# Optimization experiments

Hardware: AMD Instinct MI355X
Metric: run time of the kernel (lower is better)

Reference implementation:

```python
import jax, jax.numpy as jnp
import numpy as np


def ste_sign(x):
    # larq ste_sign forward: sign(x) with sign(0) = 1
    return jnp.where(x >= 0, 1.0, -1.0).astype(x.dtype)


def setup_inputs() -> dict:
    key = jax.random.key(0)
    ks = jax.random.split(key, 8)
    B, H, W, Cin, Cout = 32, 56, 56, 256, 256
    x = jax.random.normal(ks[0], (B, H, W, Cin), dtype=jnp.float32)
    bias1 = jax.random.normal(ks[1], (1, 1, 1, Cin), dtype=jnp.float32) * 0.01
    kernel = jax.random.normal(ks[2], (3, 3, Cin, Cout), dtype=jnp.float32) * 0.1
    # BatchNormalization(scale=False): beta learnable, gamma=1, moving stats
    bn_beta = jax.random.normal(ks[3], (Cout,), dtype=jnp.float32) * 0.01
    bn_mean = jax.random.normal(ks[4], (Cout,), dtype=jnp.float32) * 0.01
    bn_var = jax.random.uniform(ks[5], (Cout,), dtype=jnp.float32, minval=0.5, maxval=1.5)
    bias2 = jax.random.normal(ks[6], (1, 1, 1, Cout), dtype=jnp.float32) * 0.01
    return {"x": x, "bias1": bias1, "kernel": kernel, "bn_beta": bn_beta,
            "bn_mean": bn_mean, "bn_var": bn_var, "bias2": bias2}


def reference(x, bias1, kernel, bn_beta, bn_mean, bn_var, bias2):
    eps = 1e-3  # keras BatchNormalization default epsilon
    strides = 1
    # lb_activation_1: learnable bias + ste_sign activation
    a = ste_sign(x + bias1)
    # QuantConv2D: binarize kernel, 'same' padding conv (NHWC, HWIO)
    qk = ste_sign(kernel)
    y = jax.lax.conv_general_dilated(
        a, qk, window_strides=(strides, strides), padding='SAME',
        dimension_numbers=('NHWC', 'HWIO', 'NHWC'))
    # BatchNormalization(scale=False) inference: (y - mean)/sqrt(var+eps) + beta
    y = (y - bn_mean) * jax.lax.rsqrt(bn_var + eps) + bn_beta
    # strides == 1: no avgpool residual branch
    # lb_activation_2: learnable bias + relu
    out = jax.nn.relu(y + bias2)
    return out
```

## Files before the change

### kernel.cpp

```cpp
#include <hip/hip_runtime.h>


typedef int v4i __attribute__((ext_vector_type(4)));
typedef unsigned int u32;

#define NB   32
#define HW   56
#define HP   58
#define HP2  (HP*HP)
#define CIN  256
#define COUT 256
#define NPIX (NB*HW*HW)
#define KTOT 2304
#define BM   128
#define BN   256
#define NSTEP 36
#define NWG  (NPIX/BM)

#define PA_BYTES ((size_t)NB*HP*HP*CIN)
#define WT_OFF   PA_BYTES
#define WT_BYTES ((size_t)KTOT*COUT)
#define SC_OFF   (WT_OFF + WT_BYTES)
#define SH_OFF   (SC_OFF + 1024)

__device__ __forceinline__ void g2l16(const void* g, void* l) {
    __builtin_amdgcn_global_load_lds(
        (const __attribute__((address_space(1))) void*)g,
        (__attribute__((address_space(3))) void*)l, 16, 0, 0);
}

__global__ __launch_bounds__(256) void pack_a_kernel(
    const float* __restrict__ x, const float* __restrict__ b1,
    signed char* __restrict__ pa)
{
    const int lane = threadIdx.x & 63;
    const int pp = blockIdx.x * 4 + (threadIdx.x >> 6);
    const int n = pp / HP2, r = pp % HP2, ph = r / HP, pw = r % HP;
    const int ci = lane * 4;
    u32 o = 0;
    if (ph >= 1 && ph <= HW && pw >= 1 && pw <= HW) {
        const int pix = (n * HW + ph - 1) * HW + (pw - 1);
        const float4 xv = *(const float4*)(x + (size_t)pix * CIN + ci);
        const float4 bv = *(const float4*)(b1 + ci);
        o  = (u32)(unsigned char)((xv.x + bv.x >= 0.f) ? 1 : -1);
        o |= (u32)(unsigned char)((xv.y + bv.y >= 0.f) ? 1 : -1) << 8;
        o |= (u32)(unsigned char)((xv.z + bv.z >= 0.f) ? 1 : -1) << 16;
        o |= (u32)(unsigned char)((xv.w + bv.w >= 0.f) ? 1 : -1) << 24;
    }
    *(u32*)(pa + (size_t)pp * CIN + ci) = o;
}

__global__ __launch_bounds__(256) void packw_kernel(
    const float* __restrict__ k, signed char* __restrict__ wt)
{
    __shared__ signed char tile[64][256];
    const int t = threadIdx.x, k0 = blockIdx.x * 64;
    for (int j = 0; j < 64; ++j)
        tile[j][t] = (k[(size_t)(k0 + j) * COUT + t] >= 0.f) ? 1 : -1;
    __syncthreads();
    u32 wd[16];
#pragma unroll
    for (int j = 0; j < 16; ++j) wd[j] = 0;
#pragma unroll
    for (int j = 0; j < 64; ++j)
        wd[j >> 2] |= ((u32)(unsigned char)tile[j][t]) << ((j & 3) * 8);
    uint4* dst = (uint4*)(wt + (size_t)t * KTOT + k0);
#pragma unroll
    for (int j = 0; j < 4; ++j)
        dst[j] = make_uint4(wd[4*j], wd[4*j+1], wd[4*j+2], wd[4*j+3]);
}

__global__ __launch_bounds__(256) void bnprep_kernel(
    const float* __restrict__ beta, const float* __restrict__ mean,
    const float* __restrict__ var, const float* __restrict__ b2,
    float* __restrict__ scale, float* __restrict__ shift)
{
    const int t = threadIdx.x;
    const float s = rsqrtf(var[t] + 1e-3f);
    scale[t] = s;
    shift[t] = beta[t] - mean[t] * s + b2[t];
}

__global__ __launch_bounds__(256, 2) void conv_mfma_kernel(
    const signed char* __restrict__ pa, const signed char* __restrict__ wt,
    const float* __restrict__ scale, const float* __restrict__ shift,
    float* __restrict__ out)
{
    __shared__ signed char L[2][24576];

    const int t = threadIdx.x, l = t & 63, v = t >> 6;
    const int swz = (blockIdx.x & 7) * (NWG / 8) + (blockIdx.x >> 3);
    const int p0 = swz * BM;

    const signed char* abase[2];
#pragma unroll
    for (int i = 0; i < 2; ++i) {
        const int q = (t >> 2) + i * 64;
        const int p = p0 + q;
        const int n = p / 3136, r = p % 3136, h = r / 56, w = r % 56;
        const int aswz = (((t & 3) ^ ((q >> 1) & 3)) << 4);
        abase[i] = pa + ((size_t)(n * HP + h) * HP + w) * CIN + aswz;
    }
    const signed char* wbase[4];
#pragma unroll
    for (int j = 0; j < 4; ++j) {
        const int r = j * 64 + (t >> 2);
        const int bswz = (((t & 3) ^ ((r >> 1) & 3)) << 4);
        wbase[j] = wt + (size_t)r * KTOT + bswz;
    }

    int aoff[8], boff[4];
#pragma unroll
    for (int pg = 0; pg < 8; ++pg) {
        const int row = pg * 16 + (l & 15);
        aoff[pg] = row * 64 + ((((l >> 4) ^ (row >> 1)) & 3) << 4);
    }
#pragma unroll
    for (int cg = 0; cg < 4; ++cg) {
        const int row = v * 64 + cg * 16 + (l & 15);
        boff[cg] = 8192 + row * 64 + ((((l >> 4) ^ (row >> 1)) & 3) << 4);
    }

    v4i acc[8][4];
#pragma unroll
    for (int i = 0; i < 8; ++i)
#pragma unroll
        for (int j = 0; j < 4; ++j) acc[i][j] = (v4i){0, 0, 0, 0};

    auto goffA = [&](int s) {
        const int tap = s >> 2, cq = s & 3;
        const int ty = tap / 3, tx = tap - ty * 3;
        return ((ty * HP + tx) << 8) + (cq << 6);
    };
    auto STAGE = [&](int buf, int s) {
        const int go = goffA(s);
        g2l16(abase[0] + go, &L[buf][v * 1024]);
        g2l16(abase[1] + go, &L[buf][4096 + v * 1024]);
#pragma unroll
        for (int j = 0; j < 4; ++j)
            g2l16(wbase[j] + (s << 6), &L[buf][8192 + j * 4096 + v * 1024]);
    };

    STAGE(0, 0);
    asm volatile("s_waitcnt vmcnt(0)" ::: "memory");
    __builtin_amdgcn_s_barrier();

#pragma unroll 1
    for (int s = 0; s < NSTEP; ++s) {
        const int cur = s & 1, nxt = cur ^ 1;
        const signed char* Lc = &L[cur][0];
        if (s + 1 < NSTEP) STAGE(nxt, s + 1);
        v4i bf0 = *(const v4i*)(Lc + boff[0]);
        v4i bf1 = *(const v4i*)(Lc + boff[1]);
        v4i bf2 = *(const v4i*)(Lc + boff[2]);
        v4i bf3 = *(const v4i*)(Lc + boff[3]);
        v4i af[8];
#pragma unroll
        for (int pg = 0; pg < 8; ++pg) af[pg] = *(const v4i*)(Lc + aoff[pg]);
        __builtin_amdgcn_s_setprio(1);
#pragma unroll
        for (int pg = 0; pg < 8; ++pg) {
            acc[pg][0] = __builtin_amdgcn_mfma_i32_16x16x64_i8(af[pg], bf0, acc[pg][0], 0, 0, 0);
            acc[pg][1] = __builtin_amdgcn_mfma_i32_16x16x64_i8(af[pg], bf1, acc[pg][1], 0, 0, 0);
            acc[pg][2] = __builtin_amdgcn_mfma_i32_16x16x64_i8(af[pg], bf2, acc[pg][2], 0, 0, 0);
            acc[pg][3] = __builtin_amdgcn_mfma_i32_16x16x64_i8(af[pg], bf3, acc[pg][3], 0, 0, 0);
        }
        __builtin_amdgcn_s_setprio(0);
        asm volatile("s_waitcnt vmcnt(0)" ::: "memory");
        __builtin_amdgcn_s_barrier();
    }

#pragma unroll
    for (int cg = 0; cg < 4; ++cg) {
        const int co = v * 64 + cg * 16 + (l & 15);
        const float sc = scale[co], sh = shift[co];
#pragma unroll
        for (int pg = 0; pg < 8; ++pg) {
            const int prow0 = p0 + pg * 16 + (l >> 4) * 4;
#pragma unroll
            for (int rr = 0; rr < 4; ++rr) {
                const float y = (float)acc[pg][cg][rr];
                out[(size_t)(prow0 + rr) * COUT + co] = fmaxf(fmaf(y, sc, sh), 0.f);
            }
        }
    }
}

extern "C" void kernel_launch(void* const* d_in, const int* in_sizes, int n_in,
                              void* d_out, int out_size, void* d_ws, size_t ws_size,
                              hipStream_t stream)
{
    const float* x      = (const float*)d_in[0];
    const float* bias1  = (const float*)d_in[1];
    const float* kernel = (const float*)d_in[2];
    const float* bn_beta = (const float*)d_in[3];
    const float* bn_mean = (const float*)d_in[4];
    const float* bn_var  = (const float*)d_in[5];
    const float* bias2   = (const float*)d_in[6];
    float* out = (float*)d_out;

    signed char* pa  = (signed char*)d_ws;
    signed char* wtp = (signed char*)d_ws + WT_OFF;
    float* scale = (float*)((char*)d_ws + SC_OFF);
    float* shift = (float*)((char*)d_ws + SH_OFF);

    pack_a_kernel<<<dim3(NB * HP2 / 4), dim3(256), 0, stream>>>(x, bias1, pa);
    packw_kernel<<<dim3(KTOT / 64), dim3(256), 0, stream>>>(kernel, wtp);
    bnprep_kernel<<<dim3(1), dim3(256), 0, stream>>>(bn_beta, bn_mean, bn_var, bias2,
                                                     scale, shift);
    conv_mfma_kernel<<<dim3(NWG), dim3(256), 0, stream>>>(pa, wtp, scale, shift, out);
}
```

Measured before the change: 104.4 us.

## Enlarge conv tile to 256x256 with 8 waves and split MFMA phases with barriers

The implicit-GEMM conv workgroup now covers 256 pixels instead of 128 and uses 512 threads arranged as 2x4 waves. Each K-step stages twice as much A data and the same amount of weights into a larger LDS buffer, which halves per-pixel weight traffic. The MFMA loop is split into two halves separated by extra barriers so that LDS reads, the next-stage prefetch and MFMAs from different waves interleave. The costs are more barriers per step, fewer workgroups (392), and 64KB of LDS per block, which may limit occupancy.

```diff
diff --git a/kernel.cpp b/kernel.cpp
--- a/kernel.cpp
+++ b/kernel.cpp
@@ -12,7 +12,7 @@
 #define COUT 256
 #define NPIX (NB*HW*HW)
 #define KTOT 2304
-#define BM   128
+#define BM   256
 #define BN   256
 #define NSTEP 36
 #define NWG  (NPIX/BM)
@@ -81,30 +81,31 @@
     shift[t] = beta[t] - mean[t] * s + b2[t];
 }
 
-__global__ __launch_bounds__(256, 2) void conv_mfma_kernel(
+__global__ __launch_bounds__(512, 2) void conv_mfma_kernel(
     const signed char* __restrict__ pa, const signed char* __restrict__ wt,
     const float* __restrict__ scale, const float* __restrict__ shift,
     float* __restrict__ out)
 {
-    __shared__ signed char L[2][24576];
-
-    const int t = threadIdx.x, l = t & 63, v = t >> 6;
+    __shared__ signed char L[2][32768];
+
+    const int t = threadIdx.x, l = t & 63, w = t >> 6;
+    const int wr = w >> 2, wc = w & 3;
     const int swz = (blockIdx.x & 7) * (NWG / 8) + (blockIdx.x >> 3);
     const int p0 = swz * BM;
 
     const signed char* abase[2];
 #pragma unroll
     for (int i = 0; i < 2; ++i) {
-        const int q = (t >> 2) + i * 64;
+        const int q = (t >> 2) + i * 128;
         const int p = p0 + q;
-        const int n = p / 3136, r = p % 3136, h = r / 56, w = r % 56;
+        const int n = p / 3136, r = p % 3136, h = r / 56, ww = r % 56;
         const int aswz = (((t & 3) ^ ((q >> 1) & 3)) << 4);
-        abase[i] = pa + ((size_t)(n * HP + h) * HP + w) * CIN + aswz;
-    }
-    const signed char* wbase[4];
-#pragma unroll
-    for (int j = 0; j < 4; ++j) {
-        const int r = j * 64 + (t >> 2);
+        abase[i] = pa + ((size_t)(n * HP + h) * HP + ww) * CIN + aswz;
+    }
+    const signed char* wbase[2];
+#pragma unroll
+    for (int j = 0; j < 2; ++j) {
+        const int r = j * 128 + (t >> 2);
         const int bswz = (((t & 3) ^ ((r >> 1) & 3)) << 4);
         wbase[j] = wt + (size_t)r * KTOT + bswz;
     }
@@ -112,13 +113,13 @@
     int aoff[8], boff[4];
 #pragma unroll
     for (int pg = 0; pg < 8; ++pg) {
-        const int row = pg * 16 + (l & 15);
+        const int row = wr * 128 + pg * 16 + (l & 15);
         aoff[pg] = row * 64 + ((((l >> 4) ^ (row >> 1)) & 3) << 4);
     }
 #pragma unroll
     for (int cg = 0; cg < 4; ++cg) {
-        const int row = v * 64 + cg * 16 + (l & 15);
-        boff[cg] = 8192 + row * 64 + ((((l >> 4) ^ (row >> 1)) & 3) << 4);
+        const int row = wc * 64 + cg * 16 + (l & 15);
+        boff[cg] = 16384 + row * 64 + ((((l >> 4) ^ (row >> 1)) & 3) << 4);
     }
 
     v4i acc[8][4];
@@ -134,11 +135,10 @@
     };
     auto STAGE = [&](int buf, int s) {
         const int go = goffA(s);
-        g2l16(abase[0] + go, &L[buf][v * 1024]);
-        g2l16(abase[1] + go, &L[buf][4096 + v * 1024]);
-#pragma unroll
-        for (int j = 0; j < 4; ++j)
-            g2l16(wbase[j] + (s << 6), &L[buf][8192 + j * 4096 + v * 1024]);
+        g2l16(abase[0] + go, &L[buf][w * 1024]);
+        g2l16(abase[1] + go, &L[buf][8192 + w * 1024]);
+        g2l16(wbase[0] + (s << 6), &L[buf][16384 + w * 1024]);
+        g2l16(wbase[1] + (s << 6), &L[buf][24576 + w * 1024]);
     };
 
     STAGE(0, 0);
@@ -149,22 +149,62 @@
     for (int s = 0; s < NSTEP; ++s) {
         const int cur = s & 1, nxt = cur ^ 1;
         const signed char* Lc = &L[cur][0];
-        if (s + 1 < NSTEP) STAGE(nxt, s + 1);
+
         v4i bf0 = *(const v4i*)(Lc + boff[0]);
         v4i bf1 = *(const v4i*)(Lc + boff[1]);
         v4i bf2 = *(const v4i*)(Lc + boff[2]);
         v4i bf3 = *(const v4i*)(Lc + boff[3]);
-        v4i af[8];
-#pragma unroll
-        for (int pg = 0; pg < 8; ++pg) af[pg] = *(const v4i*)(Lc + aoff[pg]);
+        v4i af0 = *(const v4i*)(Lc + aoff[0]);
+        v4i af1 = *(const v4i*)(Lc + aoff[1]);
+        v4i af2 = *(const v4i*)(Lc + aoff[2]);
+        v4i af3 = *(const v4i*)(Lc + aoff[3]);
+        if (s + 1 < NSTEP) STAGE(nxt, s + 1);
+        asm volatile("" ::: "memory");
+        __builtin_amdgcn_s_barrier();
         __builtin_amdgcn_s_setprio(1);
-#pragma unroll
-        for (int pg = 0; pg < 8; ++pg) {
-            acc[pg][0] = __builtin_amdgcn_mfma_i32_16x16x64_i8(af[pg], bf0, acc[pg][0], 0, 0, 0);
-            acc[pg][1] = __builtin_amdgcn_mfma_i32_16x16x64_i8(af[pg], bf1, acc[pg][1], 0, 0, 0);
-            acc[pg][2] = __builtin_amdgcn_mfma_i32_16x16x64_i8(af[pg], bf2, acc[pg][2], 0, 0, 0);
-            acc[pg][3] = __builtin_amdgcn_mfma_i32_16x16x64_i8(af[pg], bf3, acc[pg][3], 0, 0, 0);
-        }
+        acc[0][0] = __builtin_amdgcn_mfma_i32_16x16x64_i8(af0, bf0, acc[0][0], 0, 0, 0);
+        acc[0][1] = __builtin_amdgcn_mfma_i32_16x16x64_i8(af0, bf1, acc[0][1], 0, 0, 0);
+        acc[0][2] = __builtin_amdgcn_mfma_i32_16x16x64_i8(af0, bf2, acc[0][2], 0, 0, 0);
+        acc[0][3] = __builtin_amdgcn_mfma_i32_16x16x64_i8(af0, bf3, acc[0][3], 0, 0, 0);
+        acc[1][0] = __builtin_amdgcn_mfma_i32_16x16x64_i8(af1, bf0, acc[1][0], 0, 0, 0);
+        acc[1][1] = __builtin_amdgcn_mfma_i32_16x16x64_i8(af1, bf1, acc[1][1], 0, 0, 0);
+        acc[1][2] = __builtin_amdgcn_mfma_i32_16x16x64_i8(af1, bf2, acc[1][2], 0, 0, 0);
+        acc[1][3] = __builtin_amdgcn_mfma_i32_16x16x64_i8(af1, bf3, acc[1][3], 0, 0, 0);
+        acc[2][0] = __builtin_amdgcn_mfma_i32_16x16x64_i8(af2, bf0, acc[2][0], 0, 0, 0);
+        acc[2][1] = __builtin_amdgcn_mfma_i32_16x16x64_i8(af2, bf1, acc[2][1], 0, 0, 0);
+        acc[2][2] = __builtin_amdgcn_mfma_i32_16x16x64_i8(af2, bf2, acc[2][2], 0, 0, 0);
+        acc[2][3] = __builtin_amdgcn_mfma_i32_16x16x64_i8(af2, bf3, acc[2][3], 0, 0, 0);
+        acc[3][0] = __builtin_amdgcn_mfma_i32_16x16x64_i8(af3, bf0, acc[3][0], 0, 0, 0);
+        acc[3][1] = __builtin_amdgcn_mfma_i32_16x16x64_i8(af3, bf1, acc[3][1], 0, 0, 0);
+        acc[3][2] = __builtin_amdgcn_mfma_i32_16x16x64_i8(af3, bf2, acc[3][2], 0, 0, 0);
+        acc[3][3] = __builtin_amdgcn_mfma_i32_16x16x64_i8(af3, bf3, acc[3][3], 0, 0, 0);
+        __builtin_amdgcn_s_setprio(0);
+        asm volatile("" ::: "memory");
+        __builtin_amdgcn_s_barrier();
+
+        v4i af4 = *(const v4i*)(Lc + aoff[4]);
+        v4i af5 = *(const v4i*)(Lc + aoff[5]);
+        v4i af6 = *(const v4i*)(Lc + aoff[6]);
+        v4i af7 = *(const v4i*)(Lc + aoff[7]);
+        asm volatile("" ::: "memory");
+        __builtin_amdgcn_s_barrier();
+        __builtin_amdgcn_s_setprio(1);
+        acc[4][0] = __builtin_amdgcn_mfma_i32_16x16x64_i8(af4, bf0, acc[4][0], 0, 0, 0);
+        acc[4][1] = __builtin_amdgcn_mfma_i32_16x16x64_i8(af4, bf1, acc[4][1], 0, 0, 0);
+        acc[4][2] = __builtin_amdgcn_mfma_i32_16x16x64_i8(af4, bf2, acc[4][2], 0, 0, 0);
+        acc[4][3] = __builtin_amdgcn_mfma_i32_16x16x64_i8(af4, bf3, acc[4][3], 0, 0, 0);
+        acc[5][0] = __builtin_amdgcn_mfma_i32_16x16x64_i8(af5, bf0, acc[5][0], 0, 0, 0);
+        acc[5][1] = __builtin_amdgcn_mfma_i32_16x16x64_i8(af5, bf1, acc[5][1], 0, 0, 0);
+        acc[5][2] = __builtin_amdgcn_mfma_i32_16x16x64_i8(af5, bf2, acc[5][2], 0, 0, 0);
+        acc[5][3] = __builtin_amdgcn_mfma_i32_16x16x64_i8(af5, bf3, acc[5][3], 0, 0, 0);
+        acc[6][0] = __builtin_amdgcn_mfma_i32_16x16x64_i8(af6, bf0, acc[6][0], 0, 0, 0);
+        acc[6][1] = __builtin_amdgcn_mfma_i32_16x16x64_i8(af6, bf1, acc[6][1], 0, 0, 0);
+        acc[6][2] = __builtin_amdgcn_mfma_i32_16x16x64_i8(af6, bf2, acc[6][2], 0, 0, 0);
+        acc[6][3] = __builtin_amdgcn_mfma_i32_16x16x64_i8(af6, bf3, acc[6][3], 0, 0, 0);
+        acc[7][0] = __builtin_amdgcn_mfma_i32_16x16x64_i8(af7, bf0, acc[7][0], 0, 0, 0);
+        acc[7][1] = __builtin_amdgcn_mfma_i32_16x16x64_i8(af7, bf1, acc[7][1], 0, 0, 0);
+        acc[7][2] = __builtin_amdgcn_mfma_i32_16x16x64_i8(af7, bf2, acc[7][2], 0, 0, 0);
+        acc[7][3] = __builtin_amdgcn_mfma_i32_16x16x64_i8(af7, bf3, acc[7][3], 0, 0, 0);
         __builtin_amdgcn_s_setprio(0);
         asm volatile("s_waitcnt vmcnt(0)" ::: "memory");
         __builtin_amdgcn_s_barrier();
@@ -172,11 +212,11 @@
 
 #pragma unroll
     for (int cg = 0; cg < 4; ++cg) {
-        const int co = v * 64 + cg * 16 + (l & 15);
+        const int co = wc * 64 + cg * 16 + (l & 15);
         const float sc = scale[co], sh = shift[co];
 #pragma unroll
         for (int pg = 0; pg < 8; ++pg) {
-            const int prow0 = p0 + pg * 16 + (l >> 4) * 4;
+            const int prow0 = p0 + wr * 128 + pg * 16 + (l >> 4) * 4;
 #pragma unroll
             for (int rr = 0; rr < 4; ++rr) {
                 const float y = (float)acc[pg][cg][rr];
@@ -208,5 +248,5 @@
     packw_kernel<<<dim3(KTOT / 64), dim3(256), 0, stream>>>(kernel, wtp);
     bnprep_kernel<<<dim3(1), dim3(256), 0, stream>>>(bn_beta, bn_mean, bn_var, bias2,
                                                      scale, shift);
-    conv_mfma_kernel<<<dim3(NWG), dim3(256), 0, stream>>>(pa, wtp, scale, shift, out);
-}
+    conv_mfma_kernel<<<dim3(NWG), dim3(512), 0, stream>>>(pa, wtp, scale, shift, out);
+}
```

After: 108.5 us. 3.9% more time.
